# Kernel optimization log

Measured on AMD Instinct MI355X. Metric: run time of the kernel, lower is better.

## Reference

```python
import jax, jax.numpy as jnp
import numpy as np

N, K, H = 98, 10, 4        # landmarks, neighbors/node, heads
B, CIN, HC = 1024, 256, 64 # batch, in_channels, head_channels
NEG = -9e15


def setup_inputs() -> dict:
    key = jax.random.key(0)
    ks = jax.random.split(key, 3)
    rng = np.random.default_rng(0)
    # fixed sparsity pattern: K unique neighbors per row, row-major order
    cols2d = np.stack([np.sort(rng.choice(N, K, replace=False)) for _ in range(N)])
    rows = np.repeat(np.arange(N), K)
    cols = cols2d.reshape(-1)
    x = jax.random.normal(ks[0], (B, N, CIN), jnp.float32)
    W = jax.random.normal(ks[1], (H, 2, CIN, HC), jnp.float32) * 0.05  # xavier-ish
    e = jnp.ones((H, N * K), jnp.float32)  # nn.init.constant_(e, 1)
    stdv = 1.0 / np.sqrt(HC)
    bias = jax.random.uniform(ks[2], (H, HC), jnp.float32, -stdv, stdv)
    return {"x": x, "W": W, "e": e, "bias": bias,
            "rows": jnp.asarray(rows, jnp.int32),
            "cols": jnp.asarray(cols, jnp.int32)}


def reference(x, W, e, bias, rows, cols):
    # h0/h1 for all heads at once: [2, H, B, N, HC]
    h = jnp.einsum('bnc,hscd->shbnd', x, W)
    h0, h1 = h[0], h[1]
    # masked adjacency logits per head: -9e15 everywhere, learned e at edges
    base = jnp.full((N, N), NEG, jnp.float32)
    logits = jax.vmap(lambda eh: base.at[rows, cols].set(eh))(e)  # [H,N,N]
    A = jax.nn.softmax(logits, axis=-1)  # F.softmax(adj, dim=1) on [N,N]
    diag = jnp.diagonal(A, axis1=-2, axis2=-1)  # [H,N] -> adj*M part
    A_off = A - diag[..., None] * jnp.eye(N, dtype=A.dtype)  # adj*(1-M)
    out = diag[:, None, :, None] * h0 + jnp.einsum('hij,hbjd->hbid', A_off, h1)
    out = out + bias[:, None, None, :]  # [H,B,N,HC]
    # concat heads along channel dim -> [B, N, H*HC]
    return jnp.transpose(out, (1, 2, 0, 3)).reshape(B, N, H * HC)
```

## Files before the change

kernel.cpp:

```cpp
#include <hip/hip_runtime.h>

typedef __bf16 bf16;
typedef bf16 bf16x4 __attribute__((ext_vector_type(4)));
typedef bf16 bf16x8 __attribute__((ext_vector_type(8)));
typedef _Float16 half_t;
typedef half_t half4 __attribute__((ext_vector_type(4)));
typedef half_t half8 __attribute__((ext_vector_type(8)));
typedef float f32x4 __attribute__((ext_vector_type(4)));

#define NND 98
#define KNB 10
#define NH 4
#define CIN 256
#define HC 64
#define KAG 224
#define SROW 232
#define XA_TILE (7 * 8 * 64 * 8)

#define WP_OFF   0
#define WP_BYTES 262144
#define G2D_OFF  (WP_OFF + WP_BYTES)
#define G2D_BYTES (NH * 112 * KAG * 2)
#define G2A_OFF  (G2D_OFF + G2D_BYTES)
#define G2A_BYTES (NH * 49 * 64 * 8 * 2)
#define XA_OFF   (G2A_OFF + G2A_BYTES)

__global__ __launch_bounds__(256) void misc1_kernel(const float* __restrict__ W,
                                                    bf16* __restrict__ Wp,
                                                    const float* __restrict__ e,
                                                    const int* __restrict__ cols,
                                                    half_t* __restrict__ G2d) {
  if (blockIdx.x < 64) {
    int t = blockIdx.x * 256 + threadIdx.x;
    int lane = t & 63;
    int nt = (t >> 6) & 3;
    int kt = (t >> 8) & 7;
    int hs = t >> 11;
    int n = nt * 16 + (lane & 15);
    int kb = kt * 32 + (lane >> 4) * 8;
    const float* src = W + (hs * CIN + kb) * HC + n;
    bf16x8 v;
#pragma unroll
    for (int j = 0; j < 8; ++j) v[j] = (bf16)src[j * HC];
    *(bf16x8*)(Wp + (long long)t * 8) = v;
    return;
  }
  const int h = blockIdx.x - 64;
  half_t* g = G2d + h * 112 * KAG;
  for (int i = threadIdx.x; i < 112 * KAG / 2; i += 256) ((unsigned int*)g)[i] = 0u;
  __syncthreads();
  const int i = threadIdx.x;
  if (i < NND) {
    const int* cp = cols + i * KNB;
    const float* ep = e + (h * NND + i) * KNB;
    float ev[KNB];
    int cv[KNB];
    float mx = -3.0e38f;
#pragma unroll
    for (int j = 0; j < KNB; ++j) { cv[j] = cp[j]; ev[j] = ep[j]; mx = fmaxf(mx, ev[j]); }
    float s = 0.f;
#pragma unroll
    for (int j = 0; j < KNB; ++j) { ev[j] = __expf(ev[j] - mx); s += ev[j]; }
    const float inv = 1.f / s;
    float dg = 0.f;
#pragma unroll
    for (int j = 0; j < KNB; ++j) {
      float wj = ev[j] * inv;
      if (cv[j] == i) { dg = wj; wj = 0.f; }
      g[i * KAG + cv[j]] = (half_t)wj;
    }
    g[i * KAG + 112 + i] = (half_t)dg;
  }
}

__global__ __launch_bounds__(256) void misc2_kernel(const half_t* __restrict__ G2d,
                                                    half_t* __restrict__ G2a,
                                                    const float* __restrict__ x,
                                                    bf16* __restrict__ xa, int B) {
  if (blockIdx.x < 49) {
    int t = blockIdx.x * 256 + threadIdx.x;
    int lane = t & 63;
    int q = t >> 6;
    int kt = q % 7;
    int mt = (q / 7) % 7;
    int h = q / 49;
    int row = mt * 16 + (lane & 15);
    int k0 = kt * 32 + (lane >> 4) * 8;
    half8 v = *(const half8*)(G2d + (h * 112 + row) * KAG + k0);
    *(half8*)(G2a + (long long)t * 8) = v;
    return;
  }
  __shared__ __align__(16) bf16 xs[16 * 256];
  const int b = blockIdx.x - 49;
  const int tid = threadIdx.x;
  const float* xb = x + (long long)b * NND * CIN;
  for (int mt = 0; mt < 7; ++mt) {
#pragma unroll
    for (int it = 0; it < 4; ++it) {
      int chunk = tid + it * 256;
      int r = chunk >> 6;
      int c4 = chunk & 63;
      int g = mt * 16 + r;
      f32x4 v = {0.f, 0.f, 0.f, 0.f};
      if (g < NND) v = *(const f32x4*)(xb + g * CIN + c4 * 4);
      bf16x4 bv;
      bv[0] = (bf16)v[0]; bv[1] = (bf16)v[1]; bv[2] = (bf16)v[2]; bv[3] = (bf16)v[3];
      int byte = (r * 512 + c4 * 8) ^ ((r & 7) << 4);
      *(bf16x4*)((char*)xs + byte) = bv;
    }
    __syncthreads();
#pragma unroll
    for (int it = 0; it < 2; ++it) {
      int u = tid + it * 256;
      int kt = u >> 6;
      int lane = u & 63;
      int r = lane & 15;
      int byte = (r * 512 + kt * 64 + (lane >> 4) * 16) ^ ((r & 7) << 4);
      bf16x8 f = *(const bf16x8*)((char*)xs + byte);
      *(bf16x8*)(xa + ((((long long)b * 7 + mt) * 8 + kt) * 64 + lane) * 8) = f;
    }
    __syncthreads();
  }
}

__global__ __launch_bounds__(512, 4) void semgconv_kernel(
    const bf16* __restrict__ xa, const half_t* __restrict__ G2a,
    const bf16* __restrict__ Wp, const float* __restrict__ bias,
    float* __restrict__ out, int nwg) {
  __shared__ __align__(16) half_t S[2][64 * SROW];

  const int tid = threadIdx.x;
  const int lane = tid & 63;
  const int wv = tid >> 6;

  int n = blockIdx.x;
  int w = ((nwg & 7) == 0) ? ((n & 7) * (nwg >> 3) + (n >> 3)) : n;
  const int bp = w >> 2;
  const int h = w & 3;
  const int b0 = bp * 2;

  const int wm = wv & 3;
  const int sh = wv >> 2;
  const int mt0 = wm * 2;
  const bool has1 = (mt0 + 1 < 7);

  f32x4 acc[2][2][4] = {};
  {
    const bf16* wpl = Wp + ((long long)((h * 2 + sh) * 32) * 64 + lane) * 8;
    const bf16* ax0 = xa + (((long long)b0 * 7 + mt0) * 8 * 64 + lane) * 8;
    const bf16* ax1 = ax0 + XA_TILE;
#pragma unroll
    for (int kt = 0; kt < 8; ++kt) {
      bf16x8 a00 = *(const bf16x8*)(ax0 + kt * 512);
      bf16x8 a10 = *(const bf16x8*)(ax1 + kt * 512);
      bf16x8 a01 = {}, a11 = {};
      if (has1) {
        a01 = *(const bf16x8*)(ax0 + 4096 + kt * 512);
        a11 = *(const bf16x8*)(ax1 + 4096 + kt * 512);
      }
      bf16x8 bfr[4];
#pragma unroll
      for (int nt = 0; nt < 4; ++nt)
        bfr[nt] = *(const bf16x8*)(wpl + (long long)((kt * 4 + nt) * 64) * 8);
#pragma unroll
      for (int nt = 0; nt < 4; ++nt) {
        acc[0][0][nt] = __builtin_amdgcn_mfma_f32_16x16x32_bf16(a00, bfr[nt], acc[0][0][nt], 0, 0, 0);
        acc[1][0][nt] = __builtin_amdgcn_mfma_f32_16x16x32_bf16(a10, bfr[nt], acc[1][0][nt], 0, 0, 0);
      }
      if (has1) {
#pragma unroll
        for (int nt = 0; nt < 4; ++nt) {
          acc[0][1][nt] = __builtin_amdgcn_mfma_f32_16x16x32_bf16(a01, bfr[nt], acc[0][1][nt], 0, 0, 0);
          acc[1][1][nt] = __builtin_amdgcn_mfma_f32_16x16x32_bf16(a11, bfr[nt], acc[1][1][nt], 0, 0, 0);
        }
      }
    }
  }

  {
    const int jb = (sh ? 0 : 112) + (lane >> 4) * 4;
    const int cb = lane & 15;
#pragma unroll
    for (int it2 = 0; it2 < 2; ++it2) {
#pragma unroll
      for (int im = 0; im < 2; ++im) {
        if (mt0 + im < 7) {
          const int j0 = jb + (mt0 + im) * 16;
#pragma unroll
          for (int nt = 0; nt < 4; ++nt) {
            half4 hv;
            hv[0] = (half_t)acc[it2][im][nt][0];
            hv[1] = (half_t)acc[it2][im][nt][1];
            hv[2] = (half_t)acc[it2][im][nt][2];
            hv[3] = (half_t)acc[it2][im][nt][3];
            *(half4*)(&S[it2][(nt * 16 + cb) * SROW + j0]) = hv;
          }
        }
      }
    }
  }
  __syncthreads();

  const int it2 = wv & 1;
  const int nt2 = wv >> 1;
  f32x4 a2[7] = {};
  {
    const half_t* g2l = G2a + ((long long)h * 49 * 64 + lane) * 8;
    const half_t* sl = &S[it2][(nt2 * 16 + (lane & 15)) * SROW + (lane >> 4) * 8];
#pragma unroll
    for (int kt = 0; kt < 7; ++kt) {
      half8 bfr = *(const half8*)(sl + kt * 32);
#pragma unroll
      for (int mt = 0; mt < 7; ++mt) {
        half8 afr = *(const half8*)(g2l + (long long)(mt * 7 + kt) * 64 * 8);
        a2[mt] = __builtin_amdgcn_mfma_f32_16x16x32_f16(afr, bfr, a2[mt], 0, 0, 0);
      }
    }
  }

  {
    const int col = nt2 * 16 + (lane & 15);
    const float bs = bias[h * HC + col];
    const int r0 = (lane >> 4) * 4;
    float* ob = out + (long long)(b0 + it2) * NND * (NH * HC) + h * HC + col;
#pragma unroll
    for (int mt = 0; mt < 7; ++mt) {
#pragma unroll
      for (int r = 0; r < 4; ++r) {
        const int row = mt * 16 + r0 + r;
        if (row < NND) ob[(long long)row * (NH * HC)] = a2[mt][r] + bs;
      }
    }
  }
}

extern "C" void kernel_launch(void* const* d_in, const int* in_sizes, int n_in,
                              void* d_out, int out_size, void* d_ws, size_t ws_size,
                              hipStream_t stream) {
  const float* x    = (const float*)d_in[0];
  const float* W    = (const float*)d_in[1];
  const float* e    = (const float*)d_in[2];
  const float* bias = (const float*)d_in[3];
  const int* cols   = (const int*)d_in[5];
  float* out        = (float*)d_out;

  int B = in_sizes[0] / (NND * CIN);

  bf16* Wp    = (bf16*)((char*)d_ws + WP_OFF);
  half_t* G2d = (half_t*)((char*)d_ws + G2D_OFF);
  half_t* G2a = (half_t*)((char*)d_ws + G2A_OFF);
  bf16* xa    = (bf16*)((char*)d_ws + XA_OFF);

  misc1_kernel<<<68, 256, 0, stream>>>(W, Wp, e, cols, G2d);
  misc2_kernel<<<49 + B, 256, 0, stream>>>(G2d, G2a, x, xa, B);

  const int nwg = (B / 2) * NH;
  semgconv_kernel<<<nwg, 512, 0, stream>>>(xa, G2a, Wp, bias, out, nwg);
}
```

Measured before the change: 258.3 us.

## Stage W in LDS, retile second GEMM, and simplify x conversion

The x-to-bf16 fragment conversion no longer goes through shared memory. Each thread now loads fp32 directly and writes fragments for four batches, using more threads in flight and no barriers. The main kernel first copies the head's packed W (64KB) into LDS so waves read B fragments from LDS instead of global memory. The second GEMM is retiled so each wave covers 2 row tiles by 4 column tiles, reusing G2 fragments instead of reloading 7 per k-step. The 64KB LDS buffer may reduce occupancy and adds an extra barrier.

```diff
diff --git a/kernel.cpp b/kernel.cpp
--- a/kernel.cpp
+++ b/kernel.cpp
@@ -24,6 +24,15 @@
 #define G2A_OFF  (G2D_OFF + G2D_BYTES)
 #define G2A_BYTES (NH * 49 * 64 * 8 * 2)
 #define XA_OFF   (G2A_OFF + G2A_BYTES)
+
+__device__ __forceinline__ bf16x8 load_a8(const float* p) {
+  f32x4 u = *(const f32x4*)p;
+  f32x4 v = *(const f32x4*)(p + 4);
+  bf16x8 a;
+  a[0] = (bf16)u[0]; a[1] = (bf16)u[1]; a[2] = (bf16)u[2]; a[3] = (bf16)u[3];
+  a[4] = (bf16)v[0]; a[5] = (bf16)v[1]; a[6] = (bf16)v[2]; a[7] = (bf16)v[3];
+  return a;
+}
 
 __global__ __launch_bounds__(256) void misc1_kernel(const float* __restrict__ W,
                                                     bf16* __restrict__ Wp,
@@ -90,36 +99,28 @@
     *(half8*)(G2a + (long long)t * 8) = v;
     return;
   }
-  __shared__ __align__(16) bf16 xs[16 * 256];
-  const int b = blockIdx.x - 49;
-  const int tid = threadIdx.x;
-  const float* xb = x + (long long)b * NND * CIN;
-  for (int mt = 0; mt < 7; ++mt) {
-#pragma unroll
-    for (int it = 0; it < 4; ++it) {
-      int chunk = tid + it * 256;
-      int r = chunk >> 6;
-      int c4 = chunk & 63;
-      int g = mt * 16 + r;
-      f32x4 v = {0.f, 0.f, 0.f, 0.f};
-      if (g < NND) v = *(const f32x4*)(xb + g * CIN + c4 * 4);
-      bf16x4 bv;
-      bv[0] = (bf16)v[0]; bv[1] = (bf16)v[1]; bv[2] = (bf16)v[2]; bv[3] = (bf16)v[3];
-      int byte = (r * 512 + c4 * 8) ^ ((r & 7) << 4);
-      *(bf16x4*)((char*)xs + byte) = bv;
-    }
-    __syncthreads();
-#pragma unroll
-    for (int it = 0; it < 2; ++it) {
-      int u = tid + it * 256;
-      int kt = u >> 6;
-      int lane = u & 63;
-      int r = lane & 15;
-      int byte = (r * 512 + kt * 64 + (lane >> 4) * 16) ^ ((r & 7) << 4);
-      bf16x8 f = *(const bf16x8*)((char*)xs + byte);
-      *(bf16x8*)(xa + ((((long long)b * 7 + mt) * 8 + kt) * 64 + lane) * 8) = f;
-    }
-    __syncthreads();
+  const int Bq = (B + 3) >> 2;
+  int u = (blockIdx.x - 49) * 256 + threadIdx.x;
+  if (u >= Bq * 7 * 8 * 64) return;
+  const int lane = u & 63;
+  const int kt = (u >> 6) & 7;
+  const int v = u >> 9;
+  const int b0 = v / 7;
+  const int mt = v - b0 * 7;
+  const int row = mt * 16 + (lane & 15);
+  const int k0 = kt * 32 + (lane >> 4) * 8;
+  bf16x8 a[4];
+#pragma unroll
+  for (int q = 0; q < 4; ++q) {
+    const int b = b0 + Bq * q;
+    a[q] = bf16x8{};
+    if (b < B && row < NND) a[q] = load_a8(x + ((long long)b * NND + row) * CIN + k0);
+  }
+#pragma unroll
+  for (int q = 0; q < 4; ++q) {
+    const int b = b0 + Bq * q;
+    if (b < B)
+      *(bf16x8*)(xa + ((((long long)b * 7 + mt) * 8 + kt) * 64 + lane) * 8) = a[q];
   }
 }
 
@@ -127,7 +128,9 @@
     const bf16* __restrict__ xa, const half_t* __restrict__ G2a,
     const bf16* __restrict__ Wp, const float* __restrict__ bias,
     float* __restrict__ out, int nwg) {
-  __shared__ __align__(16) half_t S[2][64 * SROW];
+  __shared__ __align__(16) unsigned char smem[65536];
+  bf16* Wl = (bf16*)smem;
+  half_t* S = (half_t*)smem;
 
   const int tid = threadIdx.x;
   const int lane = tid & 63;
@@ -139,6 +142,17 @@
   const int h = w & 3;
   const int b0 = bp * 2;
 
+  {
+    const f32x4* src = (const f32x4*)(Wp + (long long)h * 32768);
+    f32x4* dst = (f32x4*)smem;
+#pragma unroll
+    for (int it = 0; it < 8; ++it) {
+      const int idx = tid + it * 512;
+      dst[idx] = src[idx];
+    }
+  }
+  __syncthreads();
+
   const int wm = wv & 3;
   const int sh = wv >> 2;
   const int mt0 = wm * 2;
@@ -146,7 +160,7 @@
 
   f32x4 acc[2][2][4] = {};
   {
-    const bf16* wpl = Wp + ((long long)((h * 2 + sh) * 32) * 64 + lane) * 8;
+    const bf16* wll = Wl + sh * 16384 + lane * 8;
     const bf16* ax0 = xa + (((long long)b0 * 7 + mt0) * 8 * 64 + lane) * 8;
     const bf16* ax1 = ax0 + XA_TILE;
 #pragma unroll
@@ -161,7 +175,7 @@
       bf16x8 bfr[4];
 #pragma unroll
       for (int nt = 0; nt < 4; ++nt)
-        bfr[nt] = *(const bf16x8*)(wpl + (long long)((kt * 4 + nt) * 64) * 8);
+        bfr[nt] = *(const bf16x8*)(wll + (kt * 4 + nt) * 512);
 #pragma unroll
       for (int nt = 0; nt < 4; ++nt) {
         acc[0][0][nt] = __builtin_amdgcn_mfma_f32_16x16x32_bf16(a00, bfr[nt], acc[0][0][nt], 0, 0, 0);
@@ -176,6 +190,7 @@
       }
     }
   }
+  __syncthreads();
 
   {
     const int jb = (sh ? 0 : 112) + (lane >> 4) * 4;
@@ -193,7 +208,7 @@
             hv[1] = (half_t)acc[it2][im][nt][1];
             hv[2] = (half_t)acc[it2][im][nt][2];
             hv[3] = (half_t)acc[it2][im][nt][3];
-            *(half4*)(&S[it2][(nt * 16 + cb) * SROW + j0]) = hv;
+            *(half4*)(&S[it2 * (64 * SROW) + (nt * 16 + cb) * SROW + j0]) = hv;
           }
         }
       }
@@ -202,33 +217,51 @@
   __syncthreads();
 
   const int it2 = wv & 1;
-  const int nt2 = wv >> 1;
-  f32x4 a2[7] = {};
-  {
-    const half_t* g2l = G2a + ((long long)h * 49 * 64 + lane) * 8;
-    const half_t* sl = &S[it2][(nt2 * 16 + (lane & 15)) * SROW + (lane >> 4) * 8];
+  const int wm2 = wv >> 1;
+  const int mt0b = wm2 * 2;
+  const bool has1b = (mt0b + 1 < 7);
+  f32x4 a2[2][4] = {};
+  {
+    const half_t* g2l = G2a + ((long long)(h * 49 + mt0b * 7) * 64 + lane) * 8;
+    const half_t* sl = S + it2 * (64 * SROW) + (lane & 15) * SROW + (lane >> 4) * 8;
 #pragma unroll
     for (int kt = 0; kt < 7; ++kt) {
-      half8 bfr = *(const half8*)(sl + kt * 32);
-#pragma unroll
-      for (int mt = 0; mt < 7; ++mt) {
-        half8 afr = *(const half8*)(g2l + (long long)(mt * 7 + kt) * 64 * 8);
-        a2[mt] = __builtin_amdgcn_mfma_f32_16x16x32_f16(afr, bfr, a2[mt], 0, 0, 0);
-      }
-    }
-  }
-
-  {
-    const int col = nt2 * 16 + (lane & 15);
-    const float bs = bias[h * HC + col];
+      half8 bfr[4];
+#pragma unroll
+      for (int nt = 0; nt < 4; ++nt)
+        bfr[nt] = *(const half8*)(sl + nt * 16 * SROW + kt * 32);
+      half8 af0 = *(const half8*)(g2l + (long long)kt * 512);
+      half8 af1 = {};
+      if (has1b) af1 = *(const half8*)(g2l + (long long)(7 + kt) * 512);
+#pragma unroll
+      for (int nt = 0; nt < 4; ++nt) {
+        a2[0][nt] = __builtin_amdgcn_mfma_f32_16x16x32_f16(af0, bfr[nt], a2[0][nt], 0, 0, 0);
+        if (has1b)
+          a2[1][nt] = __builtin_amdgcn_mfma_f32_16x16x32_f16(af1, bfr[nt], a2[1][nt], 0, 0, 0);
+      }
+    }
+  }
+
+  {
+    const int cb = lane & 15;
     const int r0 = (lane >> 4) * 4;
-    float* ob = out + (long long)(b0 + it2) * NND * (NH * HC) + h * HC + col;
-#pragma unroll
-    for (int mt = 0; mt < 7; ++mt) {
-#pragma unroll
-      for (int r = 0; r < 4; ++r) {
-        const int row = mt * 16 + r0 + r;
-        if (row < NND) ob[(long long)row * (NH * HC)] = a2[mt][r] + bs;
+    float bs[4];
+#pragma unroll
+    for (int nt = 0; nt < 4; ++nt) bs[nt] = bias[h * HC + nt * 16 + cb];
+    float* ob = out + (long long)(b0 + it2) * NND * (NH * HC) + h * HC + cb;
+#pragma unroll
+    for (int im = 0; im < 2; ++im) {
+      const int mt = mt0b + im;
+      if (mt < 7) {
+#pragma unroll
+        for (int r = 0; r < 4; ++r) {
+          const int row = mt * 16 + r0 + r;
+          if (row < NND) {
+#pragma unroll
+            for (int nt = 0; nt < 4; ++nt)
+              ob[(long long)row * (NH * HC) + nt * 16] = a2[im][nt][r] + bs[nt];
+          }
+        }
       }
     }
   }
@@ -252,7 +285,9 @@
   bf16* xa    = (bf16*)((char*)d_ws + XA_OFF);
 
   misc1_kernel<<<68, 256, 0, stream>>>(W, Wp, e, cols, G2d);
-  misc2_kernel<<<49 + B, 256, 0, stream>>>(G2d, G2a, x, xa, B);
+  const int Bq = (B + 3) >> 2;
+  const int xa_blocks = (Bq * 7 * 8 * 64 + 255) / 256;
+  misc2_kernel<<<49 + xa_blocks, 256, 0, stream>>>(G2d, G2a, x, xa, B);
 
   const int nwg = (B / 2) * NH;
   semgconv_kernel<<<nwg, 512, 0, stream>>>(xa, G2a, Wp, bias, out, nwg);
```

Result: faster. 243.8 us (-5.6%).
